# Optimization experiments

Measured on AMD Instinct MI355X. Metric: run time of the kernel, lower is better.

The kernel has to match this reference:

```python
import jax, jax.numpy as jnp
import numpy as np

T = 0.12  # softmax temperature


def _mlp(x, Wa, ba, Wb, bb, Wc, bc):
    # Linear -> ReLU -> (Dropout=id in eval) -> Linear -> ReLU -> Linear -> ReLU
    h = jax.nn.relu(x @ Wa + ba)
    h = jax.nn.relu(h @ Wb + bb)
    return jax.nn.relu(h @ Wc + bc)


def setup_inputs() -> dict:
    key = jax.random.key(0)
    ks = jax.random.split(key, 16)
    B, K, A, P = 2048, 64, 312, 128
    std = 0.01  # torch init: normal(0, 0.01), bias 0
    inp = {
        "v2s": jax.random.normal(ks[0], (B, A), jnp.float32),
        "tar_atts": jax.random.uniform(ks[1], (B, 1), jnp.float32),
        "sample_indices": jax.random.randint(ks[2], (B, K), 0, B),
        # CLproject[1]: 1 -> 1024 -> 2048 -> 312
        "W2a": std * jax.random.normal(ks[3], (1, 1024), jnp.float32),
        "b2a": jnp.zeros((1024,), jnp.float32),
        "W2b": std * jax.random.normal(ks[4], (1024, 2048), jnp.float32),
        "b2b": jnp.zeros((2048,), jnp.float32),
        "W2c": std * jax.random.normal(ks[5], (2048, A), jnp.float32),
        "b2c": jnp.zeros((A,), jnp.float32),
        # CLproject[0]: 312 -> 1024 -> 2048 -> 128
        "W1a": std * jax.random.normal(ks[6], (A, 1024), jnp.float32),
        "b1a": jnp.zeros((1024,), jnp.float32),
        "W1b": std * jax.random.normal(ks[7], (1024, 2048), jnp.float32),
        "b1b": jnp.zeros((2048,), jnp.float32),
        "W1c": std * jax.random.normal(ks[8], (2048, P), jnp.float32),
        "b1c": jnp.zeros((P,), jnp.float32),
    }
    return inp


def reference(v2s, tar_atts, sample_indices, W2a, b2a, W2b, b2b, W2c, b2c,
              W1a, b1a, W1b, b1b, W1c, b1c):
    # attribute embedding via CLproject[1]: [B,1] -> [B,312]
    att = _mlp(tar_atts, W2a, b2a, W2b, b2b, W2c, b2c)
    v2s_sg = jax.lax.stop_gradient(v2s)  # detach().clone()
    # gather padded pos+neg sample lists: [B,K,312]
    samples = v2s_sg[sample_indices]
    # per-sample projection via CLproject[0]
    proj_samples = _mlp(samples + att[:, None, :], W1a, b1a, W1b, b1b, W1c, b1c)  # [B,K,128]
    query = _mlp(v2s_sg + att, W1a, b1a, W1b, b1b, W1c, b1c)  # [B,128]
    # batched version of per-sample einsum('c,kc->k')
    logits = jnp.einsum("bc,bkc->bk", query, proj_samples) / T
    return logits
```

## Files before the change

kernel.cpp:

```cpp
#include <hip/hip_runtime.h>
#include <stdio.h>
#include <stdint.h>

typedef __attribute__((ext_vector_type(8))) short short8;
typedef __attribute__((ext_vector_type(4))) float f32x4;
typedef __attribute__((ext_vector_type(4))) unsigned short ushort4v;

__device__ __forceinline__ unsigned short f2bf(float f) {
  unsigned int u = __builtin_bit_cast(unsigned int, f);
  u = u + 0x7FFFu + ((u >> 16) & 1u);
  return (unsigned short)(u >> 16);
}
__device__ __forceinline__ float bf2f(unsigned short h) {
  unsigned int u = ((unsigned int)h) << 16;
  return __builtin_bit_cast(float, u);
}

__device__ __forceinline__ void gl_lds16(const unsigned short* g, unsigned short* l) {
  __builtin_amdgcn_global_load_lds(
      (const __attribute__((address_space(1))) unsigned int*)(const void*)g,
      (__attribute__((address_space(3))) unsigned int*)(void*)l, 16, 0, 0);
}

__global__ void k_transpose_cast(const float* __restrict__ in, unsigned short* __restrict__ out,
                                 int Nin, int Kin, int ldo) {
  int k = blockIdx.x * blockDim.x + threadIdx.x;
  int n = blockIdx.y;
  if (k >= ldo) return;
  float v = (n < Nin && k < Kin) ? in[(size_t)k * Nin + n] : 0.f;
  out[(size_t)n * ldo + k] = f2bf(v);
}

__global__ void k_att_l1(const float* __restrict__ tar, const float* __restrict__ W2a,
                         const float* __restrict__ b2a, unsigned short* __restrict__ out) {
  int id = blockIdx.x * 256 + threadIdx.x;
  int b = id >> 10, j = id & 1023;
  out[id] = f2bf(fmaxf(tar[b] * W2a[j] + b2a[j], 0.f));
}

__global__ void k_v2s_cast(const float* __restrict__ v2s, unsigned short* __restrict__ out) {
  int id = blockIdx.x * 256 + threadIdx.x;
  int r = id / 320, c = id - r * 320;
  out[id] = (c < 312) ? f2bf(v2s[(size_t)r * 312 + c]) : (unsigned short)0;
}

__device__ __forceinline__ int lds_off(int row, int g) {
  int slot = (g + (row >> 1)) & 3;
  return row * 32 + slot * 8;
}

template<bool RELU, bool OUTBF16>
__global__ __launch_bounds__(256)
void k_gemm_bt(const unsigned short* __restrict__ A, const unsigned short* __restrict__ B,
               const float* __restrict__ bias, int bias_n, int nNt, int N_store, int K,
               void* __restrict__ outp, int ldo, int remap) {
  __shared__ __align__(16) unsigned short As[128 * 32];
  __shared__ __align__(16) unsigned short Bs[128 * 32];
  int d = blockIdx.x, nwg = gridDim.x;
  int L = d;
  if (remap) { int q = nwg >> 3; L = (d & 7) * q + (d >> 3); }
  int mt = L / nNt, nt = L - mt * nNt;
  size_t m0 = (size_t)mt * 128, n0 = (size_t)nt * 128;
  int tid = threadIdx.x, lane = tid & 63;
  int w = tid >> 6, wr = w >> 1, wc = w & 1;
  int sr = tid >> 2;
  int gch = ((tid & 3) - (tid >> 3)) & 3;
  const unsigned short* pA0 = A + (m0 + sr) * K + gch * 8;
  const unsigned short* pA1 = pA0 + (size_t)64 * K;
  const unsigned short* pB0 = B + (n0 + sr) * K + gch * 8;
  const unsigned short* pB1 = pB0 + (size_t)64 * K;
  unsigned short* lA0 = &As[(tid & ~63) * 8];
  unsigned short* lA1 = &As[64 * 32 + (tid & ~63) * 8];
  unsigned short* lB0 = &Bs[(tid & ~63) * 8];
  unsigned short* lB1 = &Bs[64 * 32 + (tid & ~63) * 8];

  int kg = lane >> 4, l15 = lane & 15;
  int aoff = lds_off(wr * 64 + l15, kg);
  int boff = lds_off(wc * 64 + l15, kg);

  f32x4 acc[4][4];
  #pragma unroll
  for (int i = 0; i < 4; ++i)
    #pragma unroll
    for (int j = 0; j < 4; ++j) acc[i][j] = (f32x4)(0.f);

  for (int k0 = 0; k0 < K; k0 += 32) {
    __syncthreads();
    gl_lds16(pA0 + k0, lA0);
    gl_lds16(pA1 + k0, lA1);
    gl_lds16(pB0 + k0, lB0);
    gl_lds16(pB1 + k0, lB1);
    __syncthreads();
    short8 af[4], bfr[4];
    #pragma unroll
    for (int mi = 0; mi < 4; ++mi) af[mi] = *(const short8*)&As[aoff + mi * 512];
    #pragma unroll
    for (int ni = 0; ni < 4; ++ni) bfr[ni] = *(const short8*)&Bs[boff + ni * 512];
    #pragma unroll
    for (int mi = 0; mi < 4; ++mi)
      #pragma unroll
      for (int ni = 0; ni < 4; ++ni)
        acc[mi][ni] = __builtin_amdgcn_mfma_f32_16x16x32_bf16(af[mi], bfr[ni], acc[mi][ni], 0, 0, 0);
  }

  #pragma unroll
  for (int ni = 0; ni < 4; ++ni) {
    int colg = (int)n0 + wc * 64 + ni * 16 + l15;
    if (colg < N_store) {
      float bs = bias ? (colg < bias_n ? bias[colg] : 0.f) : 0.f;
      #pragma unroll
      for (int mi = 0; mi < 4; ++mi) {
        #pragma unroll
        for (int r2 = 0; r2 < 4; ++r2) {
          size_t rowg = m0 + wr * 64 + mi * 16 + kg * 4 + r2;
          float v = acc[mi][ni][r2] + bs;
          if (RELU) v = fmaxf(v, 0.f);
          if (OUTBF16) ((unsigned short*)outp)[rowg * ldo + colg] = f2bf(v);
          else         ((float*)outp)[rowg * ldo + colg] = v;
        }
      }
    }
  }
}

__global__ void k_build_h1(const float* __restrict__ V1, const float* __restrict__ A1p,
                           const int* __restrict__ idx, unsigned short* __restrict__ H1c,
                           int rbase) {
  int row = rbase + blockIdx.x;
  int src, arow;
  if (row < 2048) { src = row; arow = row; }
  else {
    int g = row - 2048; arow = g >> 6;
    int s = idx[g];
    src = s < 0 ? 0 : (s > 2047 ? 2047 : s);
  }
  int j = threadIdx.x * 4;
  float4 v = *(const float4*)(V1 + (size_t)src * 1024 + j);
  float4 a = *(const float4*)(A1p + (size_t)arow * 1024 + j);
  ushort4v o;
  o.x = f2bf(fmaxf(v.x + a.x, 0.f));
  o.y = f2bf(fmaxf(v.y + a.y, 0.f));
  o.z = f2bf(fmaxf(v.z + a.z, 0.f));
  o.w = f2bf(fmaxf(v.w + a.w, 0.f));
  *(ushort4v*)(H1c + (size_t)blockIdx.x * 1024 + j) = o;
}

__global__ void k_dot(const unsigned short* __restrict__ P, float* __restrict__ out) {
  __shared__ float q[128];
  int b = blockIdx.x, t = threadIdx.x;
  if (t < 128) q[t] = bf2f(P[(size_t)b * 128 + t]);
  __syncthreads();
  int k = t >> 2, part = t & 3;
  const unsigned short* row = P + (size_t)(2048 + b * 64 + k) * 128 + part * 32;
  const float* qp = q + part * 32;
  float s = 0.f;
  #pragma unroll
  for (int j = 0; j < 32; j += 8) {
    short8 pv = *(const short8*)(row + j);
    #pragma unroll
    for (int e = 0; e < 8; ++e)
      s += bf2f((unsigned short)pv[e]) * qp[j + e];
  }
  s += __shfl_xor(s, 1);
  s += __shfl_xor(s, 2);
  if (part == 0) out[(size_t)b * 64 + k] = s * (float)(1.0 / 0.12);
}

extern "C" void kernel_launch(void* const* d_in, const int* in_sizes, int n_in,
                              void* d_out, int out_size, void* d_ws, size_t ws_size,
                              hipStream_t stream) {
  const float* v2s = (const float*)d_in[0];
  const float* tar = (const float*)d_in[1];
  const int*   sidx = (const int*)d_in[2];
  const float* W2a = (const float*)d_in[3];
  const float* b2a = (const float*)d_in[4];
  const float* W2b = (const float*)d_in[5];
  const float* b2b = (const float*)d_in[6];
  const float* W2c = (const float*)d_in[7];
  const float* b2c = (const float*)d_in[8];
  const float* W1a = (const float*)d_in[9];
  const float* b1a = (const float*)d_in[10];
  const float* W1b = (const float*)d_in[11];
  const float* b1b = (const float*)d_in[12];
  const float* W1c = (const float*)d_in[13];
  const float* b1c = (const float*)d_in[14];
  float* out = (float*)d_out;

  char* ws = (char*)d_ws;
  size_t off = 0;
  auto alloc = [&](size_t bytes) -> char* {
    char* p = ws + off; off += (bytes + 255) & ~(size_t)255; return p;
  };
  unsigned short* W1bT = (unsigned short*)alloc(2048ull * 1024 * 2);
  unsigned short* W1cT = (unsigned short*)alloc(128ull * 2048 * 2);
  float*          V1   = (float*)alloc(2048ull * 1024 * 4);
  float*          A1p  = (float*)alloc(2048ull * 1024 * 4);
  unsigned short* Pb   = (unsigned short*)alloc(133120ull * 128 * 2);
  size_t O = off;
  off = O;
  unsigned short* W1aT = (unsigned short*)alloc(1024ull * 320 * 2);
  unsigned short* v2sb = (unsigned short*)alloc(2048ull * 320 * 2);
  unsigned short* attb = (unsigned short*)alloc(2048ull * 320 * 2);
  unsigned short* W2bT = (unsigned short*)alloc(2048ull * 1024 * 2);
  unsigned short* W2cT = (unsigned short*)alloc(384ull * 2048 * 2);
  unsigned short* h_a  = (unsigned short*)alloc(2048ull * 1024 * 2);
  unsigned short* h2a  = (unsigned short*)alloc(2048ull * 2048 * 2);
  size_t early_end = off;

  const int cands[5] = {1, 2, 4, 8, 16};
  int NCH = -1, R = 0;
  size_t needed = 0;
  for (int ci = 0; ci < 5; ++ci) {
    int c = cands[ci];
    size_t Rr = 133120ull / c;
    size_t late = O + (((Rr * 1024 * 2) + 255) & ~(size_t)255)
                    + (((Rr * 2048 * 2) + 255) & ~(size_t)255);
    size_t need = late > early_end ? late : early_end;
    if (need <= ws_size) { NCH = c; R = (int)Rr; needed = need; break; }
  }
  fprintf(stderr, "[kernel_launch] ws_size=%zu NCH=%d needed=%zu\n", ws_size, NCH, needed);
  if (NCH < 0) {
    hipMemsetAsync(d_out, 0, (size_t)out_size * 4, stream);
    return;
  }
  off = O;
  unsigned short* H1c = (unsigned short*)alloc((size_t)R * 1024 * 2);
  unsigned short* H2c = (unsigned short*)alloc((size_t)R * 2048 * 2);

  dim3 blk(256);
  k_transpose_cast<<<dim3(4, 2048), blk, 0, stream>>>(W2b, W2bT, 2048, 1024, 1024);
  k_transpose_cast<<<dim3(8, 384),  blk, 0, stream>>>(W2c, W2cT, 312, 2048, 2048);
  k_transpose_cast<<<dim3(2, 1024), blk, 0, stream>>>(W1a, W1aT, 1024, 312, 320);
  k_transpose_cast<<<dim3(4, 2048), blk, 0, stream>>>(W1b, W1bT, 2048, 1024, 1024);
  k_transpose_cast<<<dim3(8, 128),  blk, 0, stream>>>(W1c, W1cT, 128, 2048, 2048);
  k_att_l1<<<8192, blk, 0, stream>>>(tar, W2a, b2a, h_a);
  k_v2s_cast<<<2560, blk, 0, stream>>>(v2s, v2sb);
  k_gemm_bt<true,  true ><<<256, blk, 0, stream>>>(h_a,  W2bT, b2b, 2048, 16, 2048, 1024, h2a,  2048, 1);
  k_gemm_bt<true,  true ><<<48,  blk, 0, stream>>>(h2a,  W2cT, b2c, 312,  3,  320,  2048, attb, 320,  1);
  k_gemm_bt<false, false><<<128, blk, 0, stream>>>(v2sb, W1aT, nullptr, 0,  8, 1024, 320, V1,  1024, 1);
  k_gemm_bt<false, false><<<128, blk, 0, stream>>>(attb, W1aT, b1a, 1024,  8, 1024, 320, A1p, 1024, 1);
  for (int c = 0; c < NCH; ++c) {
    int rbase = c * R;
    k_build_h1<<<R, blk, 0, stream>>>(V1, A1p, sidx, H1c, rbase);
    k_gemm_bt<true, true><<<(R / 128) * 16, blk, 0, stream>>>(H1c, W1bT, b1b, 2048, 16, 2048, 1024, H2c, 2048, 1);
    k_gemm_bt<true, true><<<(R / 128), blk, 0, stream>>>(H2c, W1cT, b1c, 128, 1, 128, 2048,
                                                          Pb + (size_t)rbase * 128, 128, 0);
  }
  k_dot<<<2048, blk, 0, stream>>>(Pb, out);
}
```

Measured before the change: 1.173 ms.

## Double-buffer GEMM LDS loads, tile weight transposes, and re-plan row chunking

The GEMM main loop now uses two LDS buffers. It issues the next k-tile's global-to-LDS loads before computing the current one, which removes one barrier per iteration and overlaps loads with MFMA work. The weight transpose-cast kernel now goes through a 64x64 shared-memory tile so both reads and writes are coalesced. Row chunking for the big per-sample MLP switches to plans whose chunks are multiples of 256 rows, sized to the workspace, so the GEMM grids divide evenly. Double buffering doubles LDS use per block, and with a single barrier per iteration the correctness of the overlap depends on how the async LDS loads are ordered against that barrier.

```diff
diff --git a/kernel.cpp b/kernel.cpp
--- a/kernel.cpp
+++ b/kernel.cpp
@@ -22,13 +22,37 @@
       (__attribute__((address_space(3))) unsigned int*)(void*)l, 16, 0, 0);
 }
 
-__global__ void k_transpose_cast(const float* __restrict__ in, unsigned short* __restrict__ out,
-                                 int Nin, int Kin, int ldo) {
-  int k = blockIdx.x * blockDim.x + threadIdx.x;
-  int n = blockIdx.y;
-  if (k >= ldo) return;
-  float v = (n < Nin && k < Kin) ? in[(size_t)k * Nin + n] : 0.f;
-  out[(size_t)n * ldo + k] = f2bf(v);
+__global__ void k_transpose_cast_t(const float* __restrict__ in, unsigned short* __restrict__ out,
+                                   int Nin, int Kin, int ldo) {
+  __shared__ float lds[64][65];
+  int k0 = blockIdx.x * 64, n0 = blockIdx.y * 64;
+  int t = threadIdx.x, tc = t & 15, tr = t >> 4;
+  #pragma unroll
+  for (int rr = 0; rr < 4; ++rr) {
+    int kl = tr + rr * 16, k = k0 + kl;
+    #pragma unroll
+    for (int j = 0; j < 4; ++j) {
+      int nl = tc * 4 + j, n = n0 + nl;
+      lds[kl][nl] = (k < Kin && n < Nin) ? in[(size_t)k * Nin + n] : 0.f;
+    }
+  }
+  __syncthreads();
+  #pragma unroll
+  for (int rr = 0; rr < 4; ++rr) {
+    int nl = tr + rr * 16, n = n0 + nl;
+    int kb = k0 + tc * 4;
+    if (kb + 3 < ldo) {
+      ushort4v o;
+      o.x = f2bf(lds[tc * 4 + 0][nl]);
+      o.y = f2bf(lds[tc * 4 + 1][nl]);
+      o.z = f2bf(lds[tc * 4 + 2][nl]);
+      o.w = f2bf(lds[tc * 4 + 3][nl]);
+      *(ushort4v*)&out[(size_t)n * ldo + kb] = o;
+    } else {
+      for (int j = 0; j < 4; ++j)
+        if (kb + j < ldo) out[(size_t)n * ldo + kb + j] = f2bf(lds[tc * 4 + j][nl]);
+    }
+  }
 }
 
 __global__ void k_att_l1(const float* __restrict__ tar, const float* __restrict__ W2a,
@@ -54,8 +78,8 @@
 void k_gemm_bt(const unsigned short* __restrict__ A, const unsigned short* __restrict__ B,
                const float* __restrict__ bias, int bias_n, int nNt, int N_store, int K,
                void* __restrict__ outp, int ldo, int remap) {
-  __shared__ __align__(16) unsigned short As[128 * 32];
-  __shared__ __align__(16) unsigned short Bs[128 * 32];
+  __shared__ __align__(16) unsigned short As[2][4096];
+  __shared__ __align__(16) unsigned short Bs[2][4096];
   int d = blockIdx.x, nwg = gridDim.x;
   int L = d;
   if (remap) { int q = nwg >> 3; L = (d & 7) * q + (d >> 3); }
@@ -69,10 +93,7 @@
   const unsigned short* pA1 = pA0 + (size_t)64 * K;
   const unsigned short* pB0 = B + (n0 + sr) * K + gch * 8;
   const unsigned short* pB1 = pB0 + (size_t)64 * K;
-  unsigned short* lA0 = &As[(tid & ~63) * 8];
-  unsigned short* lA1 = &As[64 * 32 + (tid & ~63) * 8];
-  unsigned short* lB0 = &Bs[(tid & ~63) * 8];
-  unsigned short* lB1 = &Bs[64 * 32 + (tid & ~63) * 8];
+  int sd = (tid & ~63) * 8;
 
   int kg = lane >> 4, l15 = lane & 15;
   int aoff = lds_off(wr * 64 + l15, kg);
@@ -84,24 +105,31 @@
     #pragma unroll
     for (int j = 0; j < 4; ++j) acc[i][j] = (f32x4)(0.f);
 
-  for (int k0 = 0; k0 < K; k0 += 32) {
+  const int NT = K >> 5;
+#define STAGE(t_, b_) do { int k0_ = (t_) * 32;                       \
+    gl_lds16(pA0 + k0_, &As[b_][sd]);                                 \
+    gl_lds16(pA1 + k0_, &As[b_][2048 + sd]);                          \
+    gl_lds16(pB0 + k0_, &Bs[b_][sd]);                                 \
+    gl_lds16(pB1 + k0_, &Bs[b_][2048 + sd]);                          \
+  } while (0)
+
+  STAGE(0, 0);
+  for (int t = 0; t < NT; ++t) {
+    int b = t & 1;
     __syncthreads();
-    gl_lds16(pA0 + k0, lA0);
-    gl_lds16(pA1 + k0, lA1);
-    gl_lds16(pB0 + k0, lB0);
-    gl_lds16(pB1 + k0, lB1);
-    __syncthreads();
+    if (t + 1 < NT) STAGE(t + 1, b ^ 1);
     short8 af[4], bfr[4];
     #pragma unroll
-    for (int mi = 0; mi < 4; ++mi) af[mi] = *(const short8*)&As[aoff + mi * 512];
-    #pragma unroll
-    for (int ni = 0; ni < 4; ++ni) bfr[ni] = *(const short8*)&Bs[boff + ni * 512];
+    for (int mi = 0; mi < 4; ++mi) af[mi] = *(const short8*)&As[b][aoff + mi * 512];
+    #pragma unroll
+    for (int ni = 0; ni < 4; ++ni) bfr[ni] = *(const short8*)&Bs[b][boff + ni * 512];
     #pragma unroll
     for (int mi = 0; mi < 4; ++mi)
       #pragma unroll
       for (int ni = 0; ni < 4; ++ni)
         acc[mi][ni] = __builtin_amdgcn_mfma_f32_16x16x32_bf16(af[mi], bfr[ni], acc[mi][ni], 0, 0, 0);
   }
+#undef STAGE
 
   #pragma unroll
   for (int ni = 0; ni < 4; ++ni) {
@@ -207,44 +235,68 @@
   unsigned short* h2a  = (unsigned short*)alloc(2048ull * 2048 * 2);
   size_t early_end = off;
 
-  const int cands[5] = {1, 2, 4, 8, 16};
-  int NCH = -1, R = 0;
-  size_t needed = 0;
-  for (int ci = 0; ci < 5; ++ci) {
-    int c = cands[ci];
-    size_t Rr = 133120ull / c;
-    size_t late = O + (((Rr * 1024 * 2) + 255) & ~(size_t)255)
-                    + (((Rr * 2048 * 2) + 255) & ~(size_t)255);
+  static const int plans[4][8] = {{260,260,0,0,0,0,0,0},
+                                  {132,132,128,128,0,0,0,0},
+                                  {130,130,130,130,0,0,0,0},
+                                  {65,65,65,65,65,65,65,65}};
+  int sel = -1, maxmt = 0;
+  for (int p = 0; p < 4 && sel < 0; ++p) {
+    int mx = 0;
+    for (int i = 0; i < 8; ++i) if (plans[p][i] > mx) mx = plans[p][i];
+    size_t rows = (size_t)mx * 256;
+    size_t late = O + ((rows * 1024 * 2 + 255) & ~(size_t)255)
+                    + ((rows * 2048 * 2 + 255) & ~(size_t)255);
     size_t need = late > early_end ? late : early_end;
-    if (need <= ws_size) { NCH = c; R = (int)Rr; needed = need; break; }
-  }
-  fprintf(stderr, "[kernel_launch] ws_size=%zu NCH=%d needed=%zu\n", ws_size, NCH, needed);
-  if (NCH < 0) {
+    if (need <= ws_size) { sel = p; maxmt = mx; }
+  }
+  int fallR = 0;
+  if (sel < 0) {
+    size_t rows = 133120ull / 16;
+    size_t late = O + ((rows * 1024 * 2 + 255) & ~(size_t)255)
+                    + ((rows * 2048 * 2 + 255) & ~(size_t)255);
+    size_t need = late > early_end ? late : early_end;
+    if (need <= ws_size) fallR = (int)rows;
+  }
+  fprintf(stderr, "[kernel_launch] ws_size=%zu sel=%d\n", ws_size, sel);
+  if (sel < 0 && !fallR) {
     hipMemsetAsync(d_out, 0, (size_t)out_size * 4, stream);
     return;
   }
   off = O;
-  unsigned short* H1c = (unsigned short*)alloc((size_t)R * 1024 * 2);
-  unsigned short* H2c = (unsigned short*)alloc((size_t)R * 2048 * 2);
+  size_t bufrows = (sel >= 0) ? (size_t)maxmt * 256 : (size_t)fallR;
+  unsigned short* H1c = (unsigned short*)alloc(bufrows * 1024 * 2);
+  unsigned short* H2c = (unsigned short*)alloc(bufrows * 2048 * 2);
 
   dim3 blk(256);
-  k_transpose_cast<<<dim3(4, 2048), blk, 0, stream>>>(W2b, W2bT, 2048, 1024, 1024);
-  k_transpose_cast<<<dim3(8, 384),  blk, 0, stream>>>(W2c, W2cT, 312, 2048, 2048);
-  k_transpose_cast<<<dim3(2, 1024), blk, 0, stream>>>(W1a, W1aT, 1024, 312, 320);
-  k_transpose_cast<<<dim3(4, 2048), blk, 0, stream>>>(W1b, W1bT, 2048, 1024, 1024);
-  k_transpose_cast<<<dim3(8, 128),  blk, 0, stream>>>(W1c, W1cT, 128, 2048, 2048);
+  k_transpose_cast_t<<<dim3(16, 32), blk, 0, stream>>>(W2b, W2bT, 2048, 1024, 1024);
+  k_transpose_cast_t<<<dim3(32, 6),  blk, 0, stream>>>(W2c, W2cT, 312, 2048, 2048);
+  k_transpose_cast_t<<<dim3(5, 16),  blk, 0, stream>>>(W1a, W1aT, 1024, 312, 320);
+  k_transpose_cast_t<<<dim3(16, 32), blk, 0, stream>>>(W1b, W1bT, 2048, 1024, 1024);
+  k_transpose_cast_t<<<dim3(32, 2),  blk, 0, stream>>>(W1c, W1cT, 128, 2048, 2048);
   k_att_l1<<<8192, blk, 0, stream>>>(tar, W2a, b2a, h_a);
   k_v2s_cast<<<2560, blk, 0, stream>>>(v2s, v2sb);
   k_gemm_bt<true,  true ><<<256, blk, 0, stream>>>(h_a,  W2bT, b2b, 2048, 16, 2048, 1024, h2a,  2048, 1);
   k_gemm_bt<true,  true ><<<48,  blk, 0, stream>>>(h2a,  W2cT, b2c, 312,  3,  320,  2048, attb, 320,  1);
   k_gemm_bt<false, false><<<128, blk, 0, stream>>>(v2sb, W1aT, nullptr, 0,  8, 1024, 320, V1,  1024, 1);
   k_gemm_bt<false, false><<<128, blk, 0, stream>>>(attb, W1aT, b1a, 1024,  8, 1024, 320, A1p, 1024, 1);
-  for (int c = 0; c < NCH; ++c) {
-    int rbase = c * R;
-    k_build_h1<<<R, blk, 0, stream>>>(V1, A1p, sidx, H1c, rbase);
-    k_gemm_bt<true, true><<<(R / 128) * 16, blk, 0, stream>>>(H1c, W1bT, b1b, 2048, 16, 2048, 1024, H2c, 2048, 1);
-    k_gemm_bt<true, true><<<(R / 128), blk, 0, stream>>>(H2c, W1cT, b1c, 128, 1, 128, 2048,
-                                                          Pb + (size_t)rbase * 128, 128, 0);
+  if (sel >= 0) {
+    int rbase = 0;
+    for (int i = 0; i < 8 && plans[sel][i]; ++i) {
+      int R = plans[sel][i] * 256;
+      k_build_h1<<<R, blk, 0, stream>>>(V1, A1p, sidx, H1c, rbase);
+      k_gemm_bt<true, true><<<(R / 128) * 16, blk, 0, stream>>>(H1c, W1bT, b1b, 2048, 16, 2048, 1024, H2c, 2048, 1);
+      k_gemm_bt<true, true><<<(R / 128), blk, 0, stream>>>(H2c, W1cT, b1c, 128, 1, 128, 2048,
+                                                            Pb + (size_t)rbase * 128, 128, 0);
+      rbase += R;
+    }
+  } else {
+    for (int c = 0; c < 16; ++c) {
+      int rbase = c * fallR;
+      k_build_h1<<<fallR, blk, 0, stream>>>(V1, A1p, sidx, H1c, rbase);
+      k_gemm_bt<true, true><<<(fallR / 128) * 16, blk, 0, stream>>>(H1c, W1bT, b1b, 2048, 16, 2048, 1024, H2c, 2048, 1);
+      k_gemm_bt<true, true><<<(fallR / 128), blk, 0, stream>>>(H2c, W1cT, b1c, 128, 1, 128, 2048,
+                                                                Pb + (size_t)rbase * 128, 128, 0);
+    }
   }
   k_dot<<<2048, blk, 0, stream>>>(Pb, out);
 }
```

Measured after the change: 1.076 ms. 8.3% less time.
